# Performance work log

Hardware: AMD Instinct MI355X
Metric: run time of the kernel (lower is better)

Reference implementation:

```python
import jax, jax.numpy as jnp
import numpy as np

N_SRC, N_MID, N_DST = 200000, 50000, 10000
D = 128
E1, E2 = 800000, 160000
EPS = 1e-12  # F.normalize eps


def setup_inputs() -> dict:
    key = jax.random.key(0)
    ks = jax.random.split(key, 12)
    s = 1.0 / np.sqrt(D)
    return {
        "x": jax.random.normal(ks[0], (N_SRC, D), jnp.float32),
        "W_l1": jax.random.uniform(ks[1], (D, D), jnp.float32, -s, s),
        "b_l1": jax.random.uniform(ks[2], (D,), jnp.float32, -s, s),
        "W_r1": jax.random.uniform(ks[3], (D, D), jnp.float32, -s, s),
        "W_l2": jax.random.uniform(ks[4], (D, D), jnp.float32, -s, s),
        "b_l2": jax.random.uniform(ks[5], (D,), jnp.float32, -s, s),
        "W_r2": jax.random.uniform(ks[6], (D, D), jnp.float32, -s, s),
        "row1": jax.random.randint(ks[7], (E1,), 0, N_SRC, jnp.int32),
        "col1": jax.random.randint(ks[8], (E1,), 0, N_MID, jnp.int32),
        "row2": jax.random.randint(ks[9], (E2,), 0, N_MID, jnp.int32),
        "col2": jax.random.randint(ks[10], (E2,), 0, N_DST, jnp.int32),
    }


def _sage_conv(x_src, x_dst, row, col, W_l, b_l, W_r, n_dst):
    # mean aggregation of source features over incoming edges (gather + scatter-add)
    msg = x_src[row]                                              # [E, D]
    agg = jax.ops.segment_sum(msg, col, num_segments=n_dst)       # [n_dst, D]
    deg = jax.ops.segment_sum(jnp.ones((row.shape[0],), x_src.dtype), col,
                              num_segments=n_dst)[:, None]        # [n_dst, 1]
    mean = jnp.where(deg > 0, agg / jnp.maximum(deg, 1.0), 0.0)
    out = mean @ W_l.T + b_l + x_dst @ W_r.T                      # lin_l + lin_r (root)
    # L2 normalize (normalize=True)
    norm = jnp.sqrt(jnp.sum(out * out, axis=-1, keepdims=True))
    return out / jnp.maximum(norm, EPS)


def reference(x, W_l1, b_l1, W_r1, W_l2, b_l2, W_r2, row1, col1, row2, col2):
    # layer 1: src = all sampled nodes, dst = first N_MID nodes
    h = _sage_conv(x, x[:N_MID], row1, col1, W_l1, b_l1, W_r1, N_MID)
    h = jax.nn.relu(h)  # dropout is identity in eval mode
    # layer 2: src = mid nodes, dst = first N_DST nodes (the batch targets)
    out = _sage_conv(h, h[:N_DST], row2, col2, W_l2, b_l2, W_r2, N_DST)
    return out
```

## Files before the change

kernel.cpp:

```cpp
#include <hip/hip_runtime.h>
#include <hip/hip_bf16.h>

#define DD 128
#define N_SRC 200000
#define N_MID 50000
#define N_DST 10000
#define E1 800000
#define E2 160000
#define CAP 64

typedef unsigned short u16;
typedef unsigned int u32;
typedef __attribute__((ext_vector_type(8))) short s16x8;
typedef __attribute__((ext_vector_type(4))) float f32x4;


__device__ __forceinline__ float bf_lo(u32 u) {
    union { u32 u; float f; } v; v.u = u << 16; return v.f;
}
__device__ __forceinline__ float bf_hi(u32 u) {
    union { u32 u; float f; } v; v.u = u & 0xffff0000u; return v.f;
}
__device__ __forceinline__ u32 f2bf_bits(float f) {
    union { float f; u32 u; } v; v.f = f;
    return (v.u + 0x7fffu + ((v.u >> 16) & 1u)) >> 16;
}
__device__ __forceinline__ u32 pack2bf(float lo, float hi) {
    return f2bf_bits(lo) | (f2bf_bits(hi) << 16);
}


#define NCONV8 (N_SRC * DD / 8)
#define WTF_T 8192
#define PREP_T (NCONV8 + WTF_T + N_MID + N_DST)

__global__ void prep_all(const float* __restrict__ x, u16* __restrict__ xb,
                         const float* __restrict__ Wl1, const float* __restrict__ Wr1,
                         u16* __restrict__ WTf1,
                         const float* __restrict__ Wl2, const float* __restrict__ Wr2,
                         u16* __restrict__ WTf2,
                         int* __restrict__ cnt1, int* __restrict__ cnt2) {
    int i = blockIdx.x * 256 + threadIdx.x;
    if (i < NCONV8) {
        const float4* x4 = (const float4*)x;
        float4 a = x4[i * 2], b = x4[i * 2 + 1];
        uint4 o;
        o.x = pack2bf(a.x, a.y); o.y = pack2bf(a.z, a.w);
        o.z = pack2bf(b.x, b.y); o.w = pack2bf(b.z, b.w);
        ((uint4*)xb)[i] = o;
    } else if (i < NCONV8 + WTF_T) {
        int t = i - NCONV8;
        int layer = t >> 12;
        int rem = t & 4095;
        int kt = rem >> 9;
        int nt = (rem >> 6) & 7;
        int lane = rem & 63;
        int gn = nt * 16 + (lane & 15);
        int k0 = kt * 32 + (lane >> 4) * 8;
        const float* Wl = layer ? Wl2 : Wl1;
        const float* Wr = layer ? Wr2 : Wr1;
        u16* WTf = layer ? WTf2 : WTf1;
        u32 o[4];
        #pragma unroll
        for (int p = 0; p < 4; ++p) {
            int ka = k0 + 2 * p, kb = ka + 1;
            float ea = (ka < 128) ? Wl[gn * 128 + ka] : Wr[gn * 128 + (ka - 128)];
            float eb = (kb < 128) ? Wl[gn * 128 + kb] : Wr[gn * 128 + (kb - 128)];
            o[p] = pack2bf(ea, eb);
        }
        ((uint4*)WTf)[(kt * 8 + nt) * 64 + lane] = make_uint4(o[0], o[1], o[2], o[3]);
    } else {
        int j = i - (NCONV8 + WTF_T);
        if (j < N_MID) cnt1[j] = 0;
        else if (j < N_MID + N_DST) cnt2[j - N_MID] = 0;
    }
}


__global__ void fill_shard(const int* __restrict__ row1, const int* __restrict__ col1,
                           const int* __restrict__ row2, const int* __restrict__ col2,
                           int* __restrict__ cnt1, int* __restrict__ cnt2,
                           int* __restrict__ csr1, int* __restrict__ csr2) {
    int b = blockIdx.x, tid = threadIdx.x;
    if (b < 1024) {
        int slice = b >> 3, shard = b & 7;
        int e0 = slice * 6250, e1 = e0 + 6250;
        for (int e = e0 + tid; e < e1; e += 256) {
            int c = col1[e];
            if (c / 6250 == shard) {
                int p = atomicAdd(&cnt1[c], 1);
                if (p < CAP) csr1[(c << 6) + p] = row1[e];
            }
        }
    } else {
        int bb = b - 1024;
        int slice = bb >> 3, shard = bb & 7;
        int e0 = slice * 10000, e1 = e0 + 10000;
        for (int e = e0 + tid; e < e1; e += 256) {
            int c = col2[e];
            if (c / 1250 == shard) {
                int p = atomicAdd(&cnt2[c], 1);
                if (p < CAP) csr2[(c << 6) + p] = row2[e];
            }
        }
    }
}


template <int ROWS, bool RELU, int MINB>
__global__ __launch_bounds__(256, MINB) void sage_kernel(
    const u16* __restrict__ xsrc_b, const u16* __restrict__ xdst_b,
    const int* __restrict__ cnt, const int* __restrict__ csrf,
    const u16* __restrict__ WTf, const float* __restrict__ bias,
    float* __restrict__ out_f, u16* __restrict__ out_b,
    int n_dst, int fp32lim)
{
    __shared__ float smem[ROWS * 132];
    const int tid = threadIdx.x;
    const int i0 = blockIdx.x * ROWS;
    const int lane = tid & 63;
    const int w = tid >> 6;
    const int quarter = lane >> 4;
    const int l16 = lane & 15;
    const int half = lane >> 5;
    const int l32 = lane & 31;
    constexpr int RPW = ROWS / 4;

    const uint4* __restrict__ xs4 = (const uint4*)xsrc_b;
    const uint2* __restrict__ xd2 = (const uint2*)xdst_b;
    uint4* sA4 = (uint4*)smem;
    uint2* sA2 = (uint2*)smem;

    for (int q = 0; q < RPW; ++q) {
        int r = w * RPW + q;
        int i = i0 + r;
        if (i < n_dst) {
            int deg = cnt[i];
            if (deg > CAP) deg = CAP;
            float acc[8] = {0.f, 0.f, 0.f, 0.f, 0.f, 0.f, 0.f, 0.f};
            if (deg > 0) {
                const int* bp = csrf + ((size_t)i << 6);
                int iv = bp[lane < deg ? lane : deg - 1];
                for (int g = 0; g < deg; g += 16) {
                    #pragma unroll
                    for (int j = 0; j < 4; ++j) {
                        if (g + 4 * j < deg) {
                            int rel = g + 4 * j + quarter;
                            int idx = __shfl(iv, rel & 63);
                            float m = (rel < deg) ? 1.f : 0.f;
                            uint4 u = xs4[(size_t)idx * 16 + l16];
                            acc[0] += m * bf_lo(u.x); acc[1] += m * bf_hi(u.x);
                            acc[2] += m * bf_lo(u.y); acc[3] += m * bf_hi(u.y);
                            acc[4] += m * bf_lo(u.z); acc[5] += m * bf_hi(u.z);
                            acc[6] += m * bf_lo(u.w); acc[7] += m * bf_hi(u.w);
                        }
                    }
                }
                #pragma unroll
                for (int k = 0; k < 8; ++k) {
                    acc[k] += __shfl_xor(acc[k], 16);
                    acc[k] += __shfl_xor(acc[k], 32);
                }
            }
            float s = (deg > 0) ? 1.f / (float)deg : 0.f;
            if (quarter == 0) {
                uint4 o;
                o.x = pack2bf(acc[0] * s, acc[1] * s);
                o.y = pack2bf(acc[2] * s, acc[3] * s);
                o.z = pack2bf(acc[4] * s, acc[5] * s);
                o.w = pack2bf(acc[6] * s, acc[7] * s);
                sA4[r * 33 + l16] = o;
            }
            if (half == 1) {
                sA2[r * 66 + 32 + l32] = xd2[(size_t)i * 32 + l32];
            }
        } else {
            if (quarter == 0) sA4[r * 33 + l16] = make_uint4(0, 0, 0, 0);
            if (half == 1)    sA2[r * 66 + 32 + l32] = make_uint2(0, 0);
        }
    }
    __syncthreads();

    constexpr int MT = ROWS / 16;
    const int nt0 = w * 2;
    const s16x8* sAv = (const s16x8*)smem;
    const s16x8* Bv = (const s16x8*)WTf;

    f32x4 C[MT][2];
    #pragma unroll
    for (int mt = 0; mt < MT; ++mt)
        #pragma unroll
        for (int ni = 0; ni < 2; ++ni)
            C[mt][ni] = (f32x4){0.f, 0.f, 0.f, 0.f};

    #pragma unroll
    for (int kt = 0; kt < 8; ++kt) {
        s16x8 a[MT];
        #pragma unroll
        for (int mt = 0; mt < MT; ++mt)
            a[mt] = sAv[(mt * 16 + l16) * 33 + kt * 4 + quarter];
        s16x8 b0 = Bv[(kt * 8 + nt0) * 64 + lane];
        s16x8 b1 = Bv[(kt * 8 + nt0 + 1) * 64 + lane];
        #pragma unroll
        for (int mt = 0; mt < MT; ++mt) {
            C[mt][0] = __builtin_amdgcn_mfma_f32_16x16x32_bf16(a[mt], b0, C[mt][0], 0, 0, 0);
            C[mt][1] = __builtin_amdgcn_mfma_f32_16x16x32_bf16(a[mt], b1, C[mt][1], 0, 0, 0);
        }
    }

    __syncthreads();
    float* sOut = smem;

    #pragma unroll
    for (int ni = 0; ni < 2; ++ni) {
        int col = (nt0 + ni) * 16 + l16;
        float bc = bias[col];
        #pragma unroll
        for (int mt = 0; mt < MT; ++mt) {
            #pragma unroll
            for (int r = 0; r < 4; ++r) {
                int row = mt * 16 + quarter * 4 + r;
                sOut[row * 132 + col] = C[mt][ni][r] + bc;
            }
        }
    }
    __syncthreads();

    constexpr int R = ROWS / 8;
    const int ty = tid >> 5;
    const int tx = tid & 31;
    #pragma unroll
    for (int r = 0; r < R; ++r) {
        int row = ty * R + r;
        float4 v = *(const float4*)(&sOut[row * 132 + tx * 4]);
        float s = v.x * v.x + v.y * v.y + v.z * v.z + v.w * v.w;
        #pragma unroll
        for (int off = 1; off < 32; off <<= 1) s += __shfl_xor(s, off);
        float scale = 1.f / fmaxf(sqrtf(s), 1e-12f);
        float v0 = v.x * scale, v1 = v.y * scale, v2 = v.z * scale, v3 = v.w * scale;
        if (RELU) {
            v0 = fmaxf(v0, 0.f); v1 = fmaxf(v1, 0.f);
            v2 = fmaxf(v2, 0.f); v3 = fmaxf(v3, 0.f);
        }
        int i = i0 + row;
        if (i < n_dst) {
            if (i < fp32lim)
                *(float4*)(out_f + (size_t)i * DD + tx * 4) = make_float4(v0, v1, v2, v3);
            if (out_b) {
                uint2 ob;
                ob.x = pack2bf(v0, v1);
                ob.y = pack2bf(v2, v3);
                *(uint2*)(out_b + (size_t)i * DD + tx * 4) = ob;
            }
        }
    }
}


extern "C" void kernel_launch(void* const* d_in, const int* in_sizes, int n_in,
                              void* d_out, int out_size, void* d_ws, size_t ws_size,
                              hipStream_t stream) {
    const float* x    = (const float*)d_in[0];
    const float* Wl1  = (const float*)d_in[1];
    const float* bl1  = (const float*)d_in[2];
    const float* Wr1  = (const float*)d_in[3];
    const float* Wl2  = (const float*)d_in[4];
    const float* bl2  = (const float*)d_in[5];
    const float* Wr2  = (const float*)d_in[6];
    const int* row1   = (const int*)d_in[7];
    const int* col1   = (const int*)d_in[8];
    const int* row2   = (const int*)d_in[9];
    const int* col2   = (const int*)d_in[10];
    float* out = (float*)d_out;

    char* p = (char*)d_ws;
    u16* xb    = (u16*)p;   p += (size_t)N_SRC * DD * sizeof(u16);
    u16* hb    = (u16*)p;   p += (size_t)N_MID * DD * sizeof(u16);
    u16* WTf1  = (u16*)p;   p += (size_t)256 * 128 * sizeof(u16);
    u16* WTf2  = (u16*)p;   p += (size_t)256 * 128 * sizeof(u16);
    int* cnt1  = (int*)p;   p += (size_t)(N_MID + 16) * sizeof(int);
    int* cnt2  = (int*)p;   p += (size_t)(N_DST + 16) * sizeof(int);
    int* csr1  = (int*)p;   p += (size_t)N_MID * CAP * sizeof(int);
    int* csr2  = (int*)p;   p += (size_t)N_DST * CAP * sizeof(int);

    prep_all<<<(PREP_T + 255) / 256, 256, 0, stream>>>(
        x, xb, Wl1, Wr1, WTf1, Wl2, Wr2, WTf2, cnt1, cnt2);

    fill_shard<<<1024 + 128, 256, 0, stream>>>(row1, col1, row2, col2,
                                               cnt1, cnt2, csr1, csr2);

    sage_kernel<32, true, 6><<<(N_MID + 31) / 32, 256, 0, stream>>>(
        xb, xb, cnt1, csr1, WTf1, bl1, (float*)nullptr, hb, N_MID, 0);

    sage_kernel<16, false, 6><<<(N_DST + 15) / 16, 256, 0, stream>>>(
        hb, hb, cnt2, csr2, WTf2, bl2, out, (u16*)nullptr, N_DST, N_DST);
}
```

Measured before the change: 305.6 us.

## Fuse bf16 prep and CSR fill into one kernel with vectorized edge loads

Merges the x/weight bf16 conversion kernel and the sharded CSR fill kernel into a single launch, so the memory-bound conversion can overlap with the atomic-heavy edge bucketing. Counter zeroing moves to hipMemsetAsync calls, since fill blocks can no longer rely on a prior kernel to clear them. Edge indices are read as int4 with nontemporal loads, and slices are made smaller to get more fill blocks. The two extra memset launches add some overhead, and the mix of block types may cause load imbalance.

```diff
diff --git a/kernel.cpp b/kernel.cpp
--- a/kernel.cpp
+++ b/kernel.cpp
@@ -13,6 +13,8 @@
 typedef unsigned int u32;
 typedef __attribute__((ext_vector_type(8))) short s16x8;
 typedef __attribute__((ext_vector_type(4))) float f32x4;
+typedef __attribute__((ext_vector_type(4))) int i32x4;
+typedef __attribute__((ext_vector_type(4))) float fv4;
 
 
 __device__ __forceinline__ float bf_lo(u32 u) {
@@ -30,78 +32,92 @@
 }
 
 
+#define FILL1_SLICE  4000
+#define FILL1_BLOCKS 1600
+#define FILL2_SLICE  4000
+#define FILL2_BLOCKS 320
+#define FILL_BLOCKS  (FILL1_BLOCKS + FILL2_BLOCKS)
+
 #define NCONV8 (N_SRC * DD / 8)
 #define WTF_T 8192
-#define PREP_T (NCONV8 + WTF_T + N_MID + N_DST)
-
-__global__ void prep_all(const float* __restrict__ x, u16* __restrict__ xb,
-                         const float* __restrict__ Wl1, const float* __restrict__ Wr1,
-                         u16* __restrict__ WTf1,
-                         const float* __restrict__ Wl2, const float* __restrict__ Wr2,
-                         u16* __restrict__ WTf2,
-                         int* __restrict__ cnt1, int* __restrict__ cnt2) {
-    int i = blockIdx.x * 256 + threadIdx.x;
-    if (i < NCONV8) {
-        const float4* x4 = (const float4*)x;
-        float4 a = x4[i * 2], b = x4[i * 2 + 1];
-        uint4 o;
-        o.x = pack2bf(a.x, a.y); o.y = pack2bf(a.z, a.w);
-        o.z = pack2bf(b.x, b.y); o.w = pack2bf(b.z, b.w);
-        ((uint4*)xb)[i] = o;
-    } else if (i < NCONV8 + WTF_T) {
-        int t = i - NCONV8;
-        int layer = t >> 12;
-        int rem = t & 4095;
-        int kt = rem >> 9;
-        int nt = (rem >> 6) & 7;
-        int lane = rem & 63;
-        int gn = nt * 16 + (lane & 15);
-        int k0 = kt * 32 + (lane >> 4) * 8;
-        const float* Wl = layer ? Wl2 : Wl1;
-        const float* Wr = layer ? Wr2 : Wr1;
-        u16* WTf = layer ? WTf2 : WTf1;
-        u32 o[4];
-        #pragma unroll
-        for (int p = 0; p < 4; ++p) {
-            int ka = k0 + 2 * p, kb = ka + 1;
-            float ea = (ka < 128) ? Wl[gn * 128 + ka] : Wr[gn * 128 + (ka - 128)];
-            float eb = (kb < 128) ? Wl[gn * 128 + kb] : Wr[gn * 128 + (kb - 128)];
-            o[p] = pack2bf(ea, eb);
-        }
-        ((uint4*)WTf)[(kt * 8 + nt) * 64 + lane] = make_uint4(o[0], o[1], o[2], o[3]);
+#define PREP_T (NCONV8 + WTF_T)
+#define PREP_BLOCKS ((PREP_T + 255) / 256)
+#define PF_BLOCKS (FILL_BLOCKS + PREP_BLOCKS)
+
+__global__ __launch_bounds__(256, 8) void prep_fill(
+    const float* __restrict__ x, u16* __restrict__ xb,
+    const float* __restrict__ Wl1, const float* __restrict__ Wr1,
+    u16* __restrict__ WTf1,
+    const float* __restrict__ Wl2, const float* __restrict__ Wr2,
+    u16* __restrict__ WTf2,
+    const int* __restrict__ row1, const int* __restrict__ col1,
+    const int* __restrict__ row2, const int* __restrict__ col2,
+    int* __restrict__ cnt1, int* __restrict__ cnt2,
+    int* __restrict__ csr1, int* __restrict__ csr2)
+{
+    const int b = blockIdx.x;
+    const int tid = threadIdx.x;
+
+    if (b < FILL_BLOCKS) {
+        const int* __restrict__ rowp;
+        const int* __restrict__ colp;
+        int* __restrict__ cnt;
+        int* __restrict__ csr;
+        int e0, e1, div;
+        const int shard = b & 7;
+        if (b < FILL1_BLOCKS) {
+            int slice = b >> 3;
+            e0 = slice * FILL1_SLICE; e1 = e0 + FILL1_SLICE;
+            rowp = row1; colp = col1; cnt = cnt1; csr = csr1; div = 6250;
+        } else {
+            int slice = (b - FILL1_BLOCKS) >> 3;
+            e0 = slice * FILL2_SLICE; e1 = e0 + FILL2_SLICE;
+            rowp = row2; colp = col2; cnt = cnt2; csr = csr2; div = 1250;
+        }
+        const int lo = shard * div;
+        for (int base = e0 + tid * 4; base < e1; base += 1024) {
+            i32x4 c4 = __builtin_nontemporal_load((const i32x4*)(colp + base));
+            i32x4 r4 = __builtin_nontemporal_load((const i32x4*)(rowp + base));
+            #pragma unroll
+            for (int k = 0; k < 4; ++k) {
+                int c = c4[k];
+                if ((u32)(c - lo) < (u32)div) {
+                    int p = atomicAdd(&cnt[c], 1);
+                    if (p < CAP) csr[(c << 6) + p] = r4[k];
+                }
+            }
+        }
     } else {
-        int j = i - (NCONV8 + WTF_T);
-        if (j < N_MID) cnt1[j] = 0;
-        else if (j < N_MID + N_DST) cnt2[j - N_MID] = 0;
-    }
-}
-
-
-__global__ void fill_shard(const int* __restrict__ row1, const int* __restrict__ col1,
-                           const int* __restrict__ row2, const int* __restrict__ col2,
-                           int* __restrict__ cnt1, int* __restrict__ cnt2,
-                           int* __restrict__ csr1, int* __restrict__ csr2) {
-    int b = blockIdx.x, tid = threadIdx.x;
-    if (b < 1024) {
-        int slice = b >> 3, shard = b & 7;
-        int e0 = slice * 6250, e1 = e0 + 6250;
-        for (int e = e0 + tid; e < e1; e += 256) {
-            int c = col1[e];
-            if (c / 6250 == shard) {
-                int p = atomicAdd(&cnt1[c], 1);
-                if (p < CAP) csr1[(c << 6) + p] = row1[e];
-            }
-        }
-    } else {
-        int bb = b - 1024;
-        int slice = bb >> 3, shard = bb & 7;
-        int e0 = slice * 10000, e1 = e0 + 10000;
-        for (int e = e0 + tid; e < e1; e += 256) {
-            int c = col2[e];
-            if (c / 1250 == shard) {
-                int p = atomicAdd(&cnt2[c], 1);
-                if (p < CAP) csr2[(c << 6) + p] = row2[e];
-            }
+        int i = (b - FILL_BLOCKS) * 256 + tid;
+        if (i < NCONV8) {
+            const fv4* x4 = (const fv4*)x;
+            fv4 a = __builtin_nontemporal_load(x4 + i * 2);
+            fv4 bb = __builtin_nontemporal_load(x4 + i * 2 + 1);
+            uint4 o;
+            o.x = pack2bf(a[0], a[1]); o.y = pack2bf(a[2], a[3]);
+            o.z = pack2bf(bb[0], bb[1]); o.w = pack2bf(bb[2], bb[3]);
+            ((uint4*)xb)[i] = o;
+        } else if (i < NCONV8 + WTF_T) {
+            int t = i - NCONV8;
+            int layer = t >> 12;
+            int rem = t & 4095;
+            int kt = rem >> 9;
+            int nt = (rem >> 6) & 7;
+            int lane = rem & 63;
+            int gn = nt * 16 + (lane & 15);
+            int k0 = kt * 32 + (lane >> 4) * 8;
+            const float* Wl = layer ? Wl2 : Wl1;
+            const float* Wr = layer ? Wr2 : Wr1;
+            u16* WTf = layer ? WTf2 : WTf1;
+            u32 o[4];
+            #pragma unroll
+            for (int p = 0; p < 4; ++p) {
+                int ka = k0 + 2 * p, kb = ka + 1;
+                float ea = (ka < 128) ? Wl[gn * 128 + ka] : Wr[gn * 128 + (ka - 128)];
+                float eb = (kb < 128) ? Wl[gn * 128 + kb] : Wr[gn * 128 + (kb - 128)];
+                o[p] = pack2bf(ea, eb);
+            }
+            ((uint4*)WTf)[(kt * 8 + nt) * 64 + lane] = make_uint4(o[0], o[1], o[2], o[3]);
         }
     }
 }
@@ -283,11 +299,12 @@
     int* csr1  = (int*)p;   p += (size_t)N_MID * CAP * sizeof(int);
     int* csr2  = (int*)p;   p += (size_t)N_DST * CAP * sizeof(int);
 
-    prep_all<<<(PREP_T + 255) / 256, 256, 0, stream>>>(
-        x, xb, Wl1, Wr1, WTf1, Wl2, Wr2, WTf2, cnt1, cnt2);
-
-    fill_shard<<<1024 + 128, 256, 0, stream>>>(row1, col1, row2, col2,
-                                               cnt1, cnt2, csr1, csr2);
+    hipMemsetAsync(cnt1, 0, (size_t)N_MID * sizeof(int), stream);
+    hipMemsetAsync(cnt2, 0, (size_t)N_DST * sizeof(int), stream);
+
+    prep_fill<<<PF_BLOCKS, 256, 0, stream>>>(
+        x, xb, Wl1, Wr1, WTf1, Wl2, Wr2, WTf2,
+        row1, col1, row2, col2, cnt1, cnt2, csr1, csr2);
 
     sage_kernel<32, true, 6><<<(N_MID + 31) / 32, 256, 0, stream>>>(
         xb, xb, cnt1, csr1, WTf1, bl1, (float*)nullptr, hb, N_MID, 0);
```

Result: faster. 276.7 us (-9.5%).
